# Performance work log

Measured on AMD Instinct MI355X. Metric: run time of the kernel, lower is better.

Reference implementation:

```python
import jax, jax.numpy as jnp
import numpy as np

N_NODES = 100000
N_EDGES = 6400000
N_HEADS = 8


def setup_inputs() -> dict:
    key = jax.random.key(0)
    k1, k2 = jax.random.split(key)
    edge_val = jax.random.normal(k1, (N_EDGES, N_HEADS), dtype=jnp.float32)
    row = jax.random.randint(k2, (N_EDGES,), 0, N_NODES, dtype=jnp.int64)
    return {"edge_val": edge_val, "row": row, "num_nodes": N_NODES}


def reference(edge_val, row, num_nodes):
    # Per-head rescale: torch halves edge_val until max <= 10.
    # Halving k times == multiply by 0.5**k with k = ceil(log2(max/10)) when max > 10.
    m = jnp.max(edge_val, axis=0)  # [H]
    k = jnp.where(m > 10.0, jnp.ceil(jnp.log2(jnp.maximum(m, 1e-30) / 10.0)), 0.0)
    k = jnp.maximum(k, 0.0)
    scale = jnp.power(jnp.float32(0.5), jax.lax.stop_gradient(k))  # [H]
    e = jnp.exp(edge_val * scale)  # [E, H]
    # Per-destination-node sum of exp values (spmm of ones == segment sum by row)
    node_sum = jax.ops.segment_sum(e, row, num_segments=num_nodes)  # [N, H]
    return e / node_sum[row]  # [E, H]
```

## Files before the change

### kernel.cpp

```cpp
#include <hip/hip_runtime.h>

#define NHEADS 8
#define NNODES 100000
#define SLICE_NODES 500
#define NSLICES 200
#define NCHUNK 16
#define NBLK2 512
#define SEGCAP 128
#define SEGPC (NBLK2 / NCHUNK)
#define SLICE_F (SLICE_NODES * NHEADS)
#define SIDX_CAP 3072
#define WS_NSUM_OFF 1024

typedef float f32x4 __attribute__((ext_vector_type(4)));

#define PAIRS_B ((size_t)NBLK2 * NSLICES * SEGCAP * 4)
#define PART_B ((size_t)NSLICES * NCHUNK * SLICE_F * 4)

__device__ __forceinline__ unsigned fenc(float f) {
    unsigned u = __float_as_uint(f);
    return (u & 0x80000000u) ? ~u : (u | 0x80000000u);
}
__device__ __forceinline__ float fdec(unsigned u) {
    unsigned b = (u & 0x80000000u) ? (u ^ 0x80000000u) : ~u;
    return __uint_as_float(b);
}

__global__ void kinit(unsigned* __restrict__ gmax) {
    if (threadIdx.x < NHEADS) gmax[threadIdx.x] = 0u;
}

__global__ void __launch_bounds__(512) kscat(const float4* __restrict__ ev4,
                                             const int* __restrict__ row,
                                             long long E, long long epb,
                                             unsigned* __restrict__ gmax,
                                             unsigned* __restrict__ pairs,
                                             unsigned* __restrict__ cnt) {
    __shared__ unsigned cur[NSLICES];
    for (int i = threadIdx.x; i < NSLICES; i += 512) cur[i] = 0;
    __syncthreads();

    long long e0 = (long long)blockIdx.x * epb;
    long long e1 = e0 + epb;
    if (e1 > E) e1 = E;

    const float NEG = -3.402823466e38f;
    float m8[8];
#pragma unroll
    for (int h = 0; h < 8; ++h) m8[h] = NEG;

    unsigned pbase = (unsigned)blockIdx.x * (NSLICES * SEGCAP);
    for (long long e = e0 + threadIdx.x; e < e1; e += 512) {
        int r = row[e];
        unsigned s = (unsigned)r / SLICE_NODES;
        unsigned pos = atomicAdd(&cur[s], 1u);
        if (pos < SEGCAP)
            pairs[pbase + s * SEGCAP + pos] =
                ((unsigned)e << 9) | (unsigned)(r - (int)s * SLICE_NODES);
        float4 a = ev4[e * 2];
        float4 b = ev4[e * 2 + 1];
        m8[0] = fmaxf(m8[0], a.x); m8[1] = fmaxf(m8[1], a.y);
        m8[2] = fmaxf(m8[2], a.z); m8[3] = fmaxf(m8[3], a.w);
        m8[4] = fmaxf(m8[4], b.x); m8[5] = fmaxf(m8[5], b.y);
        m8[6] = fmaxf(m8[6], b.z); m8[7] = fmaxf(m8[7], b.w);
    }
    __syncthreads();
    for (int i = threadIdx.x; i < NSLICES; i += 512)
        cnt[(unsigned)blockIdx.x * NSLICES + i] = min(cur[i], (unsigned)SEGCAP);

#pragma unroll
    for (int h = 0; h < 8; ++h) {
#pragma unroll
        for (int off = 1; off < 64; off <<= 1)
            m8[h] = fmaxf(m8[h], __shfl_xor(m8[h], off));
    }
    __shared__ float sm2[8][8];
    int wid = threadIdx.x >> 6;
    int lane = threadIdx.x & 63;
    if (lane == 0) {
#pragma unroll
        for (int h = 0; h < 8; ++h) sm2[wid][h] = m8[h];
    }
    __syncthreads();
    if (threadIdx.x < 8) {
        float v = sm2[0][threadIdx.x];
#pragma unroll
        for (int w = 1; w < 8; ++w) v = fmaxf(v, sm2[w][threadIdx.x]);
        atomicMax(&gmax[threadIdx.x], fenc(v));
    }
}

__global__ void kscale(const unsigned* __restrict__ gmax, float* __restrict__ scale) {
    int h = threadIdx.x;
    if (h < NHEADS) {
        float m = fdec(gmax[h]);
        float k = (m > 10.0f) ? ceilf(log2f(fmaxf(m, 1e-30f) / 10.0f)) : 0.0f;
        k = fmaxf(k, 0.0f);
        scale[h] = exp2f(-k);
    }
}

__global__ void __launch_bounds__(256) kproc(const unsigned* __restrict__ pairs,
                                             const unsigned* __restrict__ cnt,
                                             const float4* __restrict__ ev4,
                                             const float* __restrict__ scale,
                                             float* __restrict__ partials) {
    __shared__ unsigned hist[SLICE_NODES];
    __shared__ unsigned part[128];
    __shared__ unsigned spair[SIDX_CAP];
    __shared__ ushort sidx[SIDX_CAP];
    __shared__ unsigned segoff[SEGPC + 1];

    int s = blockIdx.x / NCHUNK;
    int c = blockIdx.x % NCHUNK;
    int tid = threadIdx.x;

    if (tid < SEGPC)
        segoff[tid + 1] = cnt[(unsigned)(c * SEGPC + tid) * NSLICES + s];
    if (tid == 0) segoff[0] = 0;
    __syncthreads();
    if (tid == 0) {
        unsigned run = 0;
        for (int k = 1; k <= SEGPC; ++k) { run += segoff[k]; segoff[k] = run; }
    }
    __syncthreads();
    unsigned K = segoff[SEGPC];
    float* op = partials + (long long)blockIdx.x * SLICE_F;

    float s8[NHEADS];
#pragma unroll
    for (int h = 0; h < NHEADS; ++h) s8[h] = scale[h];

    int w = tid >> 6, lane = tid & 63;
    if (K <= SIDX_CAP) {
        for (int i = tid; i < SLICE_NODES; i += 256) hist[i] = 0;
        __syncthreads();
        for (int k = w; k < SEGPC; k += 4) {
            unsigned ck = segoff[k + 1] - segoff[k];
            const unsigned* src = pairs +
                (size_t)(c * SEGPC + k) * (NSLICES * SEGCAP) + (size_t)s * SEGCAP;
            for (unsigned j = lane; j < ck; j += 64) {
                unsigned p = src[j];
                spair[segoff[k] + j] = p;
                atomicAdd(&hist[p & 511u], 1u);
            }
        }
        __syncthreads();
        if (tid < 125) {
            unsigned g = tid * 4, run = 0;
#pragma unroll
            for (int k = 0; k < 4; ++k) {
                unsigned v = hist[g + k];
                hist[g + k] = run;
                run += v;
            }
            part[tid] = run;
        }
        __syncthreads();
        if (tid == 0) {
            unsigned run = 0;
            for (int j = 0; j < 125; ++j) {
                unsigned v = part[j];
                part[j] = run;
                run += v;
            }
        }
        __syncthreads();
        if (tid < 125) {
            unsigned b = part[tid], g = tid * 4;
#pragma unroll
            for (int k = 0; k < 4; ++k) hist[g + k] += b;
        }
        __syncthreads();
        for (unsigned i = tid; i < K; i += 256) {
            unsigned p = spair[i];
            unsigned pos = atomicAdd(&hist[p & 511u], 1u);
            sidx[pos] = (ushort)i;
        }
        __syncthreads();
        for (int n = tid; n < SLICE_NODES; n += 256) {
            unsigned lo = (n == 0) ? 0u : hist[n - 1];
            unsigned hi = hist[n];
            float acc[8] = {0, 0, 0, 0, 0, 0, 0, 0};
            for (unsigned p = lo; p < hi; ++p) {
                long long e = (long long)(spair[sidx[p]] >> 9);
                float4 a = ev4[e * 2];
                float4 b = ev4[e * 2 + 1];
                acc[0] += expf(a.x * s8[0]); acc[1] += expf(a.y * s8[1]);
                acc[2] += expf(a.z * s8[2]); acc[3] += expf(a.w * s8[3]);
                acc[4] += expf(b.x * s8[4]); acc[5] += expf(b.y * s8[5]);
                acc[6] += expf(b.z * s8[6]); acc[7] += expf(b.w * s8[7]);
            }
            ((float4*)(op + n * NHEADS))[0] = make_float4(acc[0], acc[1], acc[2], acc[3]);
            ((float4*)(op + n * NHEADS))[1] = make_float4(acc[4], acc[5], acc[6], acc[7]);
        }
    } else {
        for (int i = tid; i < SLICE_F; i += 256) op[i] = 0.0f;
        __syncthreads();
        for (int k = w; k < SEGPC; k += 4) {
            unsigned ck = segoff[k + 1] - segoff[k];
            const unsigned* src = pairs +
                (size_t)(c * SEGPC + k) * (NSLICES * SEGCAP) + (size_t)s * SEGCAP;
            for (unsigned j = lane; j < ck; j += 64) {
                unsigned p = src[j];
                long long e = (long long)(p >> 9);
                float* dst = op + (p & 511u) * NHEADS;
                float4 a = ev4[e * 2];
                float4 b = ev4[e * 2 + 1];
                atomicAdd(dst + 0, expf(a.x * s8[0]));
                atomicAdd(dst + 1, expf(a.y * s8[1]));
                atomicAdd(dst + 2, expf(a.z * s8[2]));
                atomicAdd(dst + 3, expf(a.w * s8[3]));
                atomicAdd(dst + 4, expf(b.x * s8[4]));
                atomicAdd(dst + 5, expf(b.y * s8[5]));
                atomicAdd(dst + 6, expf(b.z * s8[6]));
                atomicAdd(dst + 7, expf(b.w * s8[7]));
            }
        }
    }
}

__global__ void __launch_bounds__(256) kred(const float4* __restrict__ partials,
                                            float4* __restrict__ nsum,
                                            int n4sum) {
    int i = blockIdx.x * blockDim.x + threadIdx.x;
    if (i >= n4sum) return;
    const int S4 = SLICE_F / 4;
    int s = i / S4;
    int l4 = i - s * S4;
    const float4* base = partials + (long long)(s * NCHUNK) * S4 + l4;
    float4 acc = base[0];
#pragma unroll
    for (int j = 1; j < NCHUNK; ++j) {
        float4 v = base[(long long)j * S4];
        acc.x += v.x; acc.y += v.y; acc.z += v.z; acc.w += v.w;
    }
    nsum[i] = acc;
}

__global__ void __launch_bounds__(256) kout(const f32x4* __restrict__ ev4,
                                            const int* __restrict__ row,
                                            const float* __restrict__ scale,
                                            const float* __restrict__ nsum,
                                            float* __restrict__ out,
                                            long long E) {
    float4 sLo = *(const float4*)scale;
    float4 sHi = *(const float4*)(scale + 4);
    long long tid = blockIdx.x * (long long)blockDim.x + threadIdx.x;
    long long stride = (long long)gridDim.x * blockDim.x;
    for (long long e = tid; e < E; e += stride) {
        int r = __builtin_nontemporal_load(&row[e]);
        f32x4 a = __builtin_nontemporal_load(&ev4[e * 2]);
        f32x4 b = __builtin_nontemporal_load(&ev4[e * 2 + 1]);
        const float4 n0 = *(const float4*)(nsum + (long long)r * NHEADS);
        const float4 n1 = *(const float4*)(nsum + (long long)r * NHEADS + 4);
        f32x4 o0, o1;
        o0.x = expf(a.x * sLo.x) / n0.x;
        o0.y = expf(a.y * sLo.y) / n0.y;
        o0.z = expf(a.z * sLo.z) / n0.z;
        o0.w = expf(a.w * sLo.w) / n0.w;
        o1.x = expf(b.x * sHi.x) / n1.x;
        o1.y = expf(b.y * sHi.y) / n1.y;
        o1.z = expf(b.z * sHi.z) / n1.z;
        o1.w = expf(b.w * sHi.w) / n1.w;
        f32x4* dst = (f32x4*)(out + e * NHEADS);
        __builtin_nontemporal_store(o0, dst);
        __builtin_nontemporal_store(o1, dst + 1);
    }
}

extern "C" void kernel_launch(void* const* d_in, const int* in_sizes, int n_in,
                              void* d_out, int out_size, void* d_ws, size_t ws_size,
                              hipStream_t stream) {
    const float* ev = (const float*)d_in[0];
    const int* row = (const int*)d_in[1];
    long long nElem = (long long)in_sizes[0];
    long long E = nElem / NHEADS;
    long long epb = (E + NBLK2 - 1) / NBLK2;

    float* ws = (float*)d_ws;
    unsigned* gmax = (unsigned*)ws;
    float* scale = ws + 8;
    float* nsum = ws + WS_NSUM_OFF;

    char* ob = (char*)d_out;
    unsigned* pairs = (unsigned*)ob;
    float* partials = (float*)(ob + PAIRS_B);
    unsigned* cnt = (unsigned*)(ob + PAIRS_B + PART_B);

    kinit<<<1, 64, 0, stream>>>(gmax);
    kscat<<<NBLK2, 512, 0, stream>>>((const float4*)ev, row, E, epb, gmax,
                                     pairs, cnt);
    kscale<<<1, 64, 0, stream>>>(gmax, scale);
    kproc<<<NSLICES * NCHUNK, 256, 0, stream>>>(pairs, cnt, (const float4*)ev,
                                                scale, partials);
    kred<<<(NNODES * NHEADS / 4 + 255) / 256, 256, 0, stream>>>(
        (const float4*)partials, (float4*)nsum, NNODES * NHEADS / 4);
    kout<<<2048, 256, 0, stream>>>((const f32x4*)ev, row, scale, nsum,
                                   (float*)d_out, E);
}
```

Baseline: 361.4 us.

## Fuse per-head max into gather pass with speculative unscaled exp and fallback fix

Removes the edge_val read from the scatter kernel by computing the per-head max inside the processing kernel, which already loads edge values. The processing pass assumes a scale of one; a new fix kernel reruns the scaled pass only when any head's scale differs from one. This saves a full streaming read of the edge values, at the cost of an extra launch and a full recompute whenever large values occur.

Measured after the change: 328.3 us. 9.2% less time.

```diff
diff --git a/kernel.cpp b/kernel.cpp
--- a/kernel.cpp
+++ b/kernel.cpp
@@ -30,10 +30,8 @@
     if (threadIdx.x < NHEADS) gmax[threadIdx.x] = 0u;
 }
 
-__global__ void __launch_bounds__(512) kscat(const float4* __restrict__ ev4,
-                                             const int* __restrict__ row,
+__global__ void __launch_bounds__(512) kscat(const int* __restrict__ row,
                                              long long E, long long epb,
-                                             unsigned* __restrict__ gmax,
                                              unsigned* __restrict__ pairs,
                                              unsigned* __restrict__ cnt) {
     __shared__ unsigned cur[NSLICES];
@@ -43,11 +41,6 @@
     long long e0 = (long long)blockIdx.x * epb;
     long long e1 = e0 + epb;
     if (e1 > E) e1 = E;
-
-    const float NEG = -3.402823466e38f;
-    float m8[8];
-#pragma unroll
-    for (int h = 0; h < 8; ++h) m8[h] = NEG;
 
     unsigned pbase = (unsigned)blockIdx.x * (NSLICES * SEGCAP);
     for (long long e = e0 + threadIdx.x; e < e1; e += 512) {
@@ -57,59 +50,25 @@
         if (pos < SEGCAP)
             pairs[pbase + s * SEGCAP + pos] =
                 ((unsigned)e << 9) | (unsigned)(r - (int)s * SLICE_NODES);
-        float4 a = ev4[e * 2];
-        float4 b = ev4[e * 2 + 1];
-        m8[0] = fmaxf(m8[0], a.x); m8[1] = fmaxf(m8[1], a.y);
-        m8[2] = fmaxf(m8[2], a.z); m8[3] = fmaxf(m8[3], a.w);
-        m8[4] = fmaxf(m8[4], b.x); m8[5] = fmaxf(m8[5], b.y);
-        m8[6] = fmaxf(m8[6], b.z); m8[7] = fmaxf(m8[7], b.w);
     }
     __syncthreads();
     for (int i = threadIdx.x; i < NSLICES; i += 512)
         cnt[(unsigned)blockIdx.x * NSLICES + i] = min(cur[i], (unsigned)SEGCAP);
-
-#pragma unroll
-    for (int h = 0; h < 8; ++h) {
-#pragma unroll
-        for (int off = 1; off < 64; off <<= 1)
-            m8[h] = fmaxf(m8[h], __shfl_xor(m8[h], off));
-    }
-    __shared__ float sm2[8][8];
-    int wid = threadIdx.x >> 6;
-    int lane = threadIdx.x & 63;
-    if (lane == 0) {
-#pragma unroll
-        for (int h = 0; h < 8; ++h) sm2[wid][h] = m8[h];
-    }
-    __syncthreads();
-    if (threadIdx.x < 8) {
-        float v = sm2[0][threadIdx.x];
-#pragma unroll
-        for (int w = 1; w < 8; ++w) v = fmaxf(v, sm2[w][threadIdx.x]);
-        atomicMax(&gmax[threadIdx.x], fenc(v));
-    }
-}
-
-__global__ void kscale(const unsigned* __restrict__ gmax, float* __restrict__ scale) {
-    int h = threadIdx.x;
-    if (h < NHEADS) {
-        float m = fdec(gmax[h]);
-        float k = (m > 10.0f) ? ceilf(log2f(fmaxf(m, 1e-30f) / 10.0f)) : 0.0f;
-        k = fmaxf(k, 0.0f);
-        scale[h] = exp2f(-k);
-    }
-}
-
-__global__ void __launch_bounds__(256) kproc(const unsigned* __restrict__ pairs,
-                                             const unsigned* __restrict__ cnt,
-                                             const float4* __restrict__ ev4,
-                                             const float* __restrict__ scale,
-                                             float* __restrict__ partials) {
+}
+
+template <bool SCALED, bool DOMAX>
+__device__ __forceinline__ void process_chunk(const unsigned* __restrict__ pairs,
+                                              const unsigned* __restrict__ cnt,
+                                              const float4* __restrict__ ev4,
+                                              const float* __restrict__ s8,
+                                              float* __restrict__ partials,
+                                              unsigned* __restrict__ gmax) {
     __shared__ unsigned hist[SLICE_NODES];
     __shared__ unsigned part[128];
     __shared__ unsigned spair[SIDX_CAP];
     __shared__ ushort sidx[SIDX_CAP];
     __shared__ unsigned segoff[SEGPC + 1];
+    __shared__ float smx[4][8];
 
     int s = blockIdx.x / NCHUNK;
     int c = blockIdx.x % NCHUNK;
@@ -127,9 +86,12 @@
     unsigned K = segoff[SEGPC];
     float* op = partials + (long long)blockIdx.x * SLICE_F;
 
-    float s8[NHEADS];
-#pragma unroll
-    for (int h = 0; h < NHEADS; ++h) s8[h] = scale[h];
+    const float NEG = -3.402823466e38f;
+    float m8[8];
+    if (DOMAX) {
+#pragma unroll
+        for (int h = 0; h < 8; ++h) m8[h] = NEG;
+    }
 
     int w = tid >> 6, lane = tid & 63;
     if (K <= SIDX_CAP) {
@@ -186,10 +148,20 @@
                 long long e = (long long)(spair[sidx[p]] >> 9);
                 float4 a = ev4[e * 2];
                 float4 b = ev4[e * 2 + 1];
-                acc[0] += expf(a.x * s8[0]); acc[1] += expf(a.y * s8[1]);
-                acc[2] += expf(a.z * s8[2]); acc[3] += expf(a.w * s8[3]);
-                acc[4] += expf(b.x * s8[4]); acc[5] += expf(b.y * s8[5]);
-                acc[6] += expf(b.z * s8[6]); acc[7] += expf(b.w * s8[7]);
+                if (DOMAX) {
+                    m8[0] = fmaxf(m8[0], a.x); m8[1] = fmaxf(m8[1], a.y);
+                    m8[2] = fmaxf(m8[2], a.z); m8[3] = fmaxf(m8[3], a.w);
+                    m8[4] = fmaxf(m8[4], b.x); m8[5] = fmaxf(m8[5], b.y);
+                    m8[6] = fmaxf(m8[6], b.z); m8[7] = fmaxf(m8[7], b.w);
+                }
+                acc[0] += expf(SCALED ? a.x * s8[0] : a.x);
+                acc[1] += expf(SCALED ? a.y * s8[1] : a.y);
+                acc[2] += expf(SCALED ? a.z * s8[2] : a.z);
+                acc[3] += expf(SCALED ? a.w * s8[3] : a.w);
+                acc[4] += expf(SCALED ? b.x * s8[4] : b.x);
+                acc[5] += expf(SCALED ? b.y * s8[5] : b.y);
+                acc[6] += expf(SCALED ? b.z * s8[6] : b.z);
+                acc[7] += expf(SCALED ? b.w * s8[7] : b.w);
             }
             ((float4*)(op + n * NHEADS))[0] = make_float4(acc[0], acc[1], acc[2], acc[3]);
             ((float4*)(op + n * NHEADS))[1] = make_float4(acc[4], acc[5], acc[6], acc[7]);
@@ -207,17 +179,86 @@
                 float* dst = op + (p & 511u) * NHEADS;
                 float4 a = ev4[e * 2];
                 float4 b = ev4[e * 2 + 1];
-                atomicAdd(dst + 0, expf(a.x * s8[0]));
-                atomicAdd(dst + 1, expf(a.y * s8[1]));
-                atomicAdd(dst + 2, expf(a.z * s8[2]));
-                atomicAdd(dst + 3, expf(a.w * s8[3]));
-                atomicAdd(dst + 4, expf(b.x * s8[4]));
-                atomicAdd(dst + 5, expf(b.y * s8[5]));
-                atomicAdd(dst + 6, expf(b.z * s8[6]));
-                atomicAdd(dst + 7, expf(b.w * s8[7]));
-            }
-        }
-    }
+                if (DOMAX) {
+                    m8[0] = fmaxf(m8[0], a.x); m8[1] = fmaxf(m8[1], a.y);
+                    m8[2] = fmaxf(m8[2], a.z); m8[3] = fmaxf(m8[3], a.w);
+                    m8[4] = fmaxf(m8[4], b.x); m8[5] = fmaxf(m8[5], b.y);
+                    m8[6] = fmaxf(m8[6], b.z); m8[7] = fmaxf(m8[7], b.w);
+                }
+                atomicAdd(dst + 0, expf(SCALED ? a.x * s8[0] : a.x));
+                atomicAdd(dst + 1, expf(SCALED ? a.y * s8[1] : a.y));
+                atomicAdd(dst + 2, expf(SCALED ? a.z * s8[2] : a.z));
+                atomicAdd(dst + 3, expf(SCALED ? a.w * s8[3] : a.w));
+                atomicAdd(dst + 4, expf(SCALED ? b.x * s8[4] : b.x));
+                atomicAdd(dst + 5, expf(SCALED ? b.y * s8[5] : b.y));
+                atomicAdd(dst + 6, expf(SCALED ? b.z * s8[6] : b.z));
+                atomicAdd(dst + 7, expf(SCALED ? b.w * s8[7] : b.w));
+            }
+        }
+    }
+
+    if (DOMAX) {
+#pragma unroll
+        for (int h = 0; h < 8; ++h) {
+#pragma unroll
+            for (int off = 1; off < 64; off <<= 1)
+                m8[h] = fmaxf(m8[h], __shfl_xor(m8[h], off));
+        }
+        if (lane == 0) {
+#pragma unroll
+            for (int h = 0; h < 8; ++h) smx[w][h] = m8[h];
+        }
+        __syncthreads();
+        if (tid < 8) {
+            float v = smx[0][tid];
+#pragma unroll
+            for (int k = 1; k < 4; ++k) v = fmaxf(v, smx[k][tid]);
+            atomicMax(&gmax[tid], fenc(v));
+        }
+    }
+}
+
+__global__ void __launch_bounds__(256) kproc(const unsigned* __restrict__ pairs,
+                                             const unsigned* __restrict__ cnt,
+                                             const float4* __restrict__ ev4,
+                                             float* __restrict__ partials,
+                                             unsigned* __restrict__ gmax) {
+    process_chunk<false, true>(pairs, cnt, ev4, nullptr, partials, gmax);
+}
+
+__global__ void kscale(const unsigned* __restrict__ gmax,
+                       float* __restrict__ scale,
+                       unsigned* __restrict__ needfix) {
+    __shared__ float ssc[NHEADS];
+    int h = threadIdx.x;
+    if (h < NHEADS) {
+        float m = fdec(gmax[h]);
+        float k = (m > 10.0f) ? ceilf(log2f(fmaxf(m, 1e-30f) / 10.0f)) : 0.0f;
+        k = fmaxf(k, 0.0f);
+        float s = exp2f(-k);
+        scale[h] = s;
+        ssc[h] = s;
+    }
+    __syncthreads();
+    if (h == 0) {
+        unsigned nf = 0;
+#pragma unroll
+        for (int i = 0; i < NHEADS; ++i) nf |= (ssc[i] != 1.0f) ? 1u : 0u;
+        *needfix = nf;
+    }
+}
+
+__global__ void __launch_bounds__(256) kfix(const unsigned* __restrict__ pairs,
+                                            const unsigned* __restrict__ cnt,
+                                            const float4* __restrict__ ev4,
+                                            const float* __restrict__ scale,
+                                            const unsigned* __restrict__ needfix,
+                                            float* __restrict__ partials) {
+    if (*needfix == 0u) return;
+    float s8[NHEADS];
+#pragma unroll
+    for (int h = 0; h < NHEADS; ++h) s8[h] = scale[h];
+    process_chunk<true, false>(pairs, cnt, ev4, s8, partials, nullptr);
 }
 
 __global__ void __launch_bounds__(256) kred(const float4* __restrict__ partials,
@@ -281,6 +322,7 @@
     float* ws = (float*)d_ws;
     unsigned* gmax = (unsigned*)ws;
     float* scale = ws + 8;
+    unsigned* needfix = (unsigned*)(ws + 16);
     float* nsum = ws + WS_NSUM_OFF;
 
     char* ob = (char*)d_out;
@@ -289,11 +331,12 @@
     unsigned* cnt = (unsigned*)(ob + PAIRS_B + PART_B);
 
     kinit<<<1, 64, 0, stream>>>(gmax);
-    kscat<<<NBLK2, 512, 0, stream>>>((const float4*)ev, row, E, epb, gmax,
-                                     pairs, cnt);
-    kscale<<<1, 64, 0, stream>>>(gmax, scale);
+    kscat<<<NBLK2, 512, 0, stream>>>(row, E, epb, pairs, cnt);
     kproc<<<NSLICES * NCHUNK, 256, 0, stream>>>(pairs, cnt, (const float4*)ev,
-                                                scale, partials);
+                                                partials, gmax);
+    kscale<<<1, 64, 0, stream>>>(gmax, scale, needfix);
+    kfix<<<NSLICES * NCHUNK, 256, 0, stream>>>(pairs, cnt, (const float4*)ev,
+                                               scale, needfix, partials);
     kred<<<(NNODES * NHEADS / 4 + 255) / 256, 256, 0, stream>>>(
         (const float4*)partials, (float4*)nsum, NNODES * NHEADS / 4);
     kout<<<2048, 256, 0, stream>>>((const f32x4*)ev, row, scale, nsum,
```
